# Kernel optimization log

Measured on AMD Instinct MI355X. Metric: run time of the kernel, lower is better.

## Reference

```python
import jax, jax.numpy as jnp
import numpy as np

N = 50000   # nodes
E = 800000  # edges (avg degree 16)
D = 64      # feature dim (input_dim == hidden_dim == output_dim for num_layer=2)
BN_EPS = 1e-5


def setup_inputs() -> dict:
    key = jax.random.key(0)
    ks = jax.random.split(key, 8)
    def lin_w(k, fan_in, fan_out):
        return jax.random.normal(k, (fan_in, fan_out), jnp.float32) / np.sqrt(fan_in).astype(np.float32)
    inp = {
        "x": jax.random.normal(ks[0], (N, D), jnp.float32),
        "edge_index": jax.random.randint(ks[1], (2, E), 0, N),
    }
    ki = 2
    for l in range(2):
        for s in ("a", "b"):
            inp[f"w{l}{s}"] = lin_w(ks[ki], D, D)
            inp[f"b{l}{s}"] = jnp.zeros((D,), jnp.float32)
            inp[f"g{l}{s}"] = jnp.ones((D,), jnp.float32)   # BN gamma
            inp[f"be{l}{s}"] = jnp.zeros((D,), jnp.float32)  # BN beta
            ki += 1
    inp["lin_w"] = lin_w(ks[6], 2 * D, D)  # JK cat of 2 layers -> 2D, final lin -> D
    inp["lin_b"] = jnp.zeros((D,), jnp.float32)
    return inp


def _bn(h, g, b):
    # BatchNorm1d in training mode: batch statistics over the node axis
    m = h.mean(axis=0)
    v = h.var(axis=0)
    return (h - m) * jax.lax.rsqrt(v + BN_EPS) * g + b


def _gin(h, src, dst, w1, b1, g1, be1, w2, b2, g2, be2):
    # GINConv with eps=0: (1+eps)*x_i + sum_{j->i} x_j, then MLP(Lin-BN-ReLU-Lin-BN-ReLU)
    agg = jax.ops.segment_sum(h[src], dst, num_segments=N) + h
    h = jax.nn.relu(_bn(agg @ w1 + b1, g1, be1))
    return jax.nn.relu(_bn(h @ w2 + b2, g2, be2))


def reference(x, edge_index, w0a, b0a, g0a, be0a, w0b, b0b, g0b, be0b,
              w1a, b1a, g1a, be1a, w1b, b1b, g1b, be1b, lin_w, lin_b):
    src, dst = edge_index[0], edge_index[1]
    h1 = _gin(x, src, dst, w0a, b0a, g0a, be0a, w0b, b0b, g0b, be0b)
    h2 = _gin(h1, src, dst, w1a, b1a, g1a, be1a, w1b, b1b, g1b, be1b)
    # JumpingKnowledge 'cat' over the conv outputs (res[1:]), then final linear
    return jnp.concatenate([h1, h2], axis=1) @ lin_w + lin_b
```

## Files before the change

kernel.cpp:

```cpp
#include <hip/hip_runtime.h>
#include <hip/hip_bf16.h>

#define NN 50000
#define NE 800000
#define BN_EPS 1e-5f
#define CHUNK 4096
#define NCH 196
#define NBK 196

typedef __attribute__((ext_vector_type(4))) float f32x4;
typedef __attribute__((ext_vector_type(8))) short s16x8;
typedef __attribute__((ext_vector_type(4))) short s16x4;

__device__ __forceinline__ float bf2f(__hip_bfloat16 v) { return __bfloat162float(v); }
__device__ __forceinline__ short f2bs(float v) {
    __hip_bfloat16 b = __float2bfloat16(v);
    return __builtin_bit_cast(short, b);
}

__global__ void prep_k(const int* __restrict__ dst, int* __restrict__ part,
                       const float* __restrict__ x, __hip_bfloat16* __restrict__ Xb,
                       const float* __restrict__ w0a, const float* __restrict__ w0b,
                       const float* __restrict__ w1a, const float* __restrict__ w1b,
                       const float* __restrict__ lw,
                       short* __restrict__ Wt0a, short* __restrict__ Wt0b,
                       short* __restrict__ Wt1a, short* __restrict__ Wt1b,
                       short* __restrict__ Wtf) {
    int b = blockIdx.x, t = threadIdx.x;
    if (b < NCH) {
        __shared__ int c[256];
        c[t] = 0;
        __syncthreads();
        int base = b * CHUNK;
        int n = NE - base; if (n > CHUNK) n = CHUNK;
        for (int i = t; i < n; i += 256) atomicAdd(&c[dst[base + i] >> 8], 1);
        __syncthreads();
        part[b * 256 + t] = c[t];
    } else if (b < 196 + 3125) {
        int i = (b - 196) * 256 + t;
        if (i < NN * 16) {
            f32x4 v = *(const f32x4*)(x + (size_t)i * 4);
            s16x4 ov;
            #pragma unroll
            for (int j = 0; j < 4; j++) ov[j] = f2bs(v[j]);
            *(s16x4*)((short*)Xb + (size_t)i * 4) = ov;
        }
    } else {
        int wb = b - 3321;
        if (wb < 4) {
            const float* W = wb == 0 ? w0a : wb == 1 ? w0b : wb == 2 ? w1a : w1b;
            short* Wt = wb == 0 ? Wt0a : wb == 1 ? Wt0b : wb == 2 ? Wt1a : Wt1b;
            for (int e = t; e < 4096; e += 256) {
                int k = e >> 6, n = e & 63;
                Wt[n * 64 + k] = f2bs(W[e]);
            }
        } else {
            for (int e = t; e < 8192; e += 256) {
                int k = e >> 6, n = e & 63;
                Wtf[n * 128 + k] = f2bs(lw[e]);
            }
        }
    }
}

__global__ void bscan_k(const int* __restrict__ part, int* __restrict__ bbase,
                        int* __restrict__ bres, int* __restrict__ off,
                        float* __restrict__ sums) {
    __shared__ int s[256];
    int t = threadIdx.x;
    int v = 0;
    for (int c = 0; c < NCH; c++) v += part[c * 256 + t];
    s[t] = v;
    __syncthreads();
    for (int d = 1; d < 256; d <<= 1) {
        int u = (t >= d) ? s[t - d] : 0;
        __syncthreads();
        s[t] += u;
        __syncthreads();
    }
    int ex = s[t] - v;
    bbase[t] = ex;
    bres[t] = ex;
    if (t == 0) { bbase[256] = NE; off[NN] = NE; }
    sums[t] = 0.f; sums[256 + t] = 0.f;
}

__global__ void bscatter_k(const int* __restrict__ src, const int* __restrict__ dst,
                           int* __restrict__ bres, int* __restrict__ ebuf) {
    __shared__ int cnt[256], loff[256], lcur[256], gst[256], sc[256];
    __shared__ int packed[CHUNK];
    int t = threadIdx.x;
    cnt[t] = 0;
    __syncthreads();
    int base = blockIdx.x * CHUNK;
    int n = NE - base; if (n > CHUNK) n = CHUNK;
    for (int i = t; i < n; i += 256) atomicAdd(&cnt[dst[base + i] >> 8], 1);
    __syncthreads();
    sc[t] = cnt[t];
    __syncthreads();
    for (int d = 1; d < 256; d <<= 1) {
        int u = (t >= d) ? sc[t - d] : 0;
        __syncthreads();
        sc[t] += u;
        __syncthreads();
    }
    loff[t] = sc[t] - cnt[t];
    lcur[t] = loff[t];
    __syncthreads();
    for (int i = t; i < n; i += 256) {
        int d = dst[base + i];
        int b = d >> 8;
        int p = atomicAdd(&lcur[b], 1);
        packed[p] = src[base + i] | ((d & 255) << 16) | (b << 24);
    }
    __syncthreads();
    if (cnt[t]) gst[t] = atomicAdd(&bres[t], cnt[t]);
    __syncthreads();
    for (int i = t; i < n; i += 256) {
        int v = packed[i];
        int b = (v >> 24) & 255;
        ebuf[gst[b] + i - loff[b]] = v & 0xFFFFFF;
    }
}

__global__ void csr_k(const int* __restrict__ bbase, const int* __restrict__ ebuf,
                      int* __restrict__ off, int* __restrict__ adj) {
    __shared__ int cnt[256], loff[256], lcur[256], sc[256];
    int b = blockIdx.x, t = threadIdx.x;
    int s0 = bbase[b], s1 = bbase[b + 1];
    int n = s1 - s0;
    cnt[t] = 0;
    __syncthreads();
    for (int i = t; i < n; i += 256) atomicAdd(&cnt[(ebuf[s0 + i] >> 16) & 255], 1);
    __syncthreads();
    sc[t] = cnt[t];
    __syncthreads();
    for (int d = 1; d < 256; d <<= 1) {
        int u = (t >= d) ? sc[t - d] : 0;
        __syncthreads();
        sc[t] += u;
        __syncthreads();
    }
    loff[t] = sc[t] - cnt[t];
    lcur[t] = loff[t];
    int node = b * 256 + t;
    if (node < NN) off[node] = s0 + loff[t];
    __syncthreads();
    for (int i = t; i < n; i += 256) {
        int v = ebuf[s0 + i];
        int p = atomicAdd(&lcur[(v >> 16) & 255], 1);
        adj[s0 + p] = v & 0xFFFF;
    }
}

__global__ void gather_k(const __hip_bfloat16* __restrict__ X,
                         const int* __restrict__ off, const int* __restrict__ adj,
                         __hip_bfloat16* __restrict__ AGG) {
    int node = blockIdx.x * 4 + (threadIdx.x >> 6);
    int lane = threadIdx.x & 63;
    if (node >= NN) return;
    float acc = bf2f(X[(size_t)node * 64 + lane]);
    int s = off[node], e = off[node + 1];
    int p = s;
    for (; p + 8 <= e; p += 8) {
        int j0 = adj[p + 0], j1 = adj[p + 1], j2 = adj[p + 2], j3 = adj[p + 3];
        int j4 = adj[p + 4], j5 = adj[p + 5], j6 = adj[p + 6], j7 = adj[p + 7];
        float v0 = bf2f(X[(size_t)j0 * 64 + lane]);
        float v1 = bf2f(X[(size_t)j1 * 64 + lane]);
        float v2 = bf2f(X[(size_t)j2 * 64 + lane]);
        float v3 = bf2f(X[(size_t)j3 * 64 + lane]);
        float v4 = bf2f(X[(size_t)j4 * 64 + lane]);
        float v5 = bf2f(X[(size_t)j5 * 64 + lane]);
        float v6 = bf2f(X[(size_t)j6 * 64 + lane]);
        float v7 = bf2f(X[(size_t)j7 * 64 + lane]);
        acc += ((v0 + v1) + (v2 + v3)) + ((v4 + v5) + (v6 + v7));
    }
    if (p + 4 <= e) {
        int j0 = adj[p + 0], j1 = adj[p + 1], j2 = adj[p + 2], j3 = adj[p + 3];
        float v0 = bf2f(X[(size_t)j0 * 64 + lane]);
        float v1 = bf2f(X[(size_t)j1 * 64 + lane]);
        float v2 = bf2f(X[(size_t)j2 * 64 + lane]);
        float v3 = bf2f(X[(size_t)j3 * 64 + lane]);
        acc += (v0 + v1) + (v2 + v3);
        p += 4;
    }
    for (; p < e; p++) acc += bf2f(X[(size_t)adj[p] * 64 + lane]);
    AGG[(size_t)node * 64 + lane] = __float2bfloat16(acc);
}


__global__ void gemm_a_k(const __hip_bfloat16* __restrict__ Ab,
                         const short* __restrict__ Wt,
                         const float* __restrict__ bias,
                         float* __restrict__ T,
                         float* __restrict__ sums) {
    __shared__ float lsum[64], lssq[64];
    int tid = threadIdx.x;
    if (tid < 64) { lsum[tid] = 0.f; lssq[tid] = 0.f; }
    __syncthreads();
    int wv = tid >> 6, L = tid & 63;
    int m = L & 15, quad = L >> 4;
    int wrow = blockIdx.x * 64 + wv * 16;
    int arow = wrow + m;
    if (arow >= NN) arow = NN - 1;
    const short* Ap = (const short*)Ab;
    s16x8 a0 = *(const s16x8*)(Ap + (size_t)arow * 64 + quad * 8);
    s16x8 a1 = *(const s16x8*)(Ap + (size_t)arow * 64 + 32 + quad * 8);
    f32x4 acc[4];
    #pragma unroll
    for (int nt = 0; nt < 4; nt++) {
        int n = nt * 16 + m;
        s16x8 b0 = *(const s16x8*)(Wt + n * 64 + quad * 8);
        s16x8 b1 = *(const s16x8*)(Wt + n * 64 + 32 + quad * 8);
        acc[nt] = (f32x4){0.f, 0.f, 0.f, 0.f};
        acc[nt] = __builtin_amdgcn_mfma_f32_16x16x32_bf16(a0, b0, acc[nt], 0, 0, 0);
        acc[nt] = __builtin_amdgcn_mfma_f32_16x16x32_bf16(a1, b1, acc[nt], 0, 0, 0);
    }
    #pragma unroll
    for (int nt = 0; nt < 4; nt++) {
        int col = nt * 16 + m;
        float bv = bias[col];
        float ps = 0.f, pq = 0.f;
        #pragma unroll
        for (int r = 0; r < 4; r++) {
            int orow = wrow + quad * 4 + r;
            if (orow < NN) {
                float v = acc[nt][r] + bv;
                T[(size_t)orow * 64 + col] = v;
                ps += v;
                pq += v * v;
            }
        }
        atomicAdd(&lsum[col], ps);
        atomicAdd(&lssq[col], pq);
    }
    __syncthreads();
    if (tid < 64) {
        atomicAdd(&sums[tid], lsum[tid]);
        atomicAdd(&sums[64 + tid], lssq[tid]);
    }
}

__global__ void gemm_bn_k(const float* __restrict__ Tin,
                          const float* __restrict__ stats,
                          const float* __restrict__ g, const float* __restrict__ be,
                          const short* __restrict__ Wt,
                          const float* __restrict__ bias,
                          float* __restrict__ T,
                          float* __restrict__ sums) {
    __shared__ float sc[64], sh[64], lsum[64], lssq[64];
    int tid = threadIdx.x;
    if (tid < 64) {
        float mm = stats[tid] * (1.0f / NN);
        float var = stats[64 + tid] * (1.0f / NN) - mm * mm;
        if (var < 0.f) var = 0.f;
        float s = g[tid] * rsqrtf(var + BN_EPS);
        sc[tid] = s;
        sh[tid] = be[tid] - mm * s;
        lsum[tid] = 0.f; lssq[tid] = 0.f;
    }
    __syncthreads();
    int wv = tid >> 6, L = tid & 63;
    int m = L & 15, quad = L >> 4;
    int wrow = blockIdx.x * 64 + wv * 16;
    int arow = wrow + m;
    if (arow >= NN) arow = NN - 1;
    f32x4 t0 = *(const f32x4*)(Tin + (size_t)arow * 64 + quad * 8);
    f32x4 t1 = *(const f32x4*)(Tin + (size_t)arow * 64 + quad * 8 + 4);
    f32x4 t2 = *(const f32x4*)(Tin + (size_t)arow * 64 + 32 + quad * 8);
    f32x4 t3 = *(const f32x4*)(Tin + (size_t)arow * 64 + 32 + quad * 8 + 4);
    s16x8 a0, a1;
    #pragma unroll
    for (int j = 0; j < 4; j++) {
        int k0 = quad * 8 + j, k1 = quad * 8 + 4 + j;
        float u0 = t0[j] * sc[k0] + sh[k0]; a0[j]     = f2bs(u0 > 0.f ? u0 : 0.f);
        float u1 = t1[j] * sc[k1] + sh[k1]; a0[4 + j] = f2bs(u1 > 0.f ? u1 : 0.f);
        float u2 = t2[j] * sc[32 + k0] + sh[32 + k0]; a1[j]     = f2bs(u2 > 0.f ? u2 : 0.f);
        float u3 = t3[j] * sc[32 + k1] + sh[32 + k1]; a1[4 + j] = f2bs(u3 > 0.f ? u3 : 0.f);
    }
    f32x4 acc[4];
    #pragma unroll
    for (int nt = 0; nt < 4; nt++) {
        int n = nt * 16 + m;
        s16x8 b0 = *(const s16x8*)(Wt + n * 64 + quad * 8);
        s16x8 b1 = *(const s16x8*)(Wt + n * 64 + 32 + quad * 8);
        acc[nt] = (f32x4){0.f, 0.f, 0.f, 0.f};
        acc[nt] = __builtin_amdgcn_mfma_f32_16x16x32_bf16(a0, b0, acc[nt], 0, 0, 0);
        acc[nt] = __builtin_amdgcn_mfma_f32_16x16x32_bf16(a1, b1, acc[nt], 0, 0, 0);
    }
    #pragma unroll
    for (int nt = 0; nt < 4; nt++) {
        int col = nt * 16 + m;
        float bv = bias[col];
        float ps = 0.f, pq = 0.f;
        #pragma unroll
        for (int r = 0; r < 4; r++) {
            int orow = wrow + quad * 4 + r;
            if (orow < NN) {
                float v = acc[nt][r] + bv;
                T[(size_t)orow * 64 + col] = v;
                ps += v;
                pq += v * v;
            }
        }
        atomicAdd(&lsum[col], ps);
        atomicAdd(&lssq[col], pq);
    }
    __syncthreads();
    if (tid < 64) {
        atomicAdd(&sums[tid], lsum[tid]);
        atomicAdd(&sums[64 + tid], lssq[tid]);
    }
}

__global__ void bn_k(const float* __restrict__ T, const float* __restrict__ sums,
                     const float* __restrict__ g, const float* __restrict__ be,
                     __hip_bfloat16* __restrict__ Hb) {
    __shared__ float sc[64], sh[64];
    int tid = threadIdx.x;
    if (tid < 64) {
        float m = sums[tid] * (1.0f / NN);
        float var = sums[64 + tid] * (1.0f / NN) - m * m;
        if (var < 0.f) var = 0.f;
        float s = g[tid] * rsqrtf(var + BN_EPS);
        sc[tid] = s;
        sh[tid] = be[tid] - m * s;
    }
    __syncthreads();
    int i = blockIdx.x * 256 + tid;
    if (i < NN * 16) {
        int row = i >> 4, f = (i & 15) * 4;
        f32x4 v = *(const f32x4*)(T + (size_t)row * 64 + f);
        s16x4 ub;
        #pragma unroll
        for (int j = 0; j < 4; j++) {
            float w = v[j] * sc[f + j] + sh[f + j];
            ub[j] = f2bs(w > 0.f ? w : 0.f);
        }
        *(s16x4*)((short*)Hb + (size_t)row * 64 + f) = ub;
    }
}

__global__ void gemm_fin_k(const __hip_bfloat16* __restrict__ H1b,
                           const float* __restrict__ T2,
                           const float* __restrict__ stats,
                           const float* __restrict__ g, const float* __restrict__ be,
                           const short* __restrict__ Wtf,
                           const float* __restrict__ bias,
                           float* __restrict__ O) {
    __shared__ float sc[64], sh[64];
    int tid = threadIdx.x;
    if (tid < 64) {
        float mm = stats[tid] * (1.0f / NN);
        float var = stats[64 + tid] * (1.0f / NN) - mm * mm;
        if (var < 0.f) var = 0.f;
        float s = g[tid] * rsqrtf(var + BN_EPS);
        sc[tid] = s;
        sh[tid] = be[tid] - mm * s;
    }
    __syncthreads();
    int wv = tid >> 6, L = tid & 63;
    int m = L & 15, quad = L >> 4;
    int wrow = blockIdx.x * 64 + wv * 16;
    int arow = wrow + m;
    if (arow >= NN) arow = NN - 1;
    const short* Hp = (const short*)H1b;
    s16x8 a0 = *(const s16x8*)(Hp + (size_t)arow * 64 + quad * 8);
    s16x8 a1 = *(const s16x8*)(Hp + (size_t)arow * 64 + 32 + quad * 8);
    f32x4 t0 = *(const f32x4*)(T2 + (size_t)arow * 64 + quad * 8);
    f32x4 t1 = *(const f32x4*)(T2 + (size_t)arow * 64 + quad * 8 + 4);
    f32x4 t2 = *(const f32x4*)(T2 + (size_t)arow * 64 + 32 + quad * 8);
    f32x4 t3 = *(const f32x4*)(T2 + (size_t)arow * 64 + 32 + quad * 8 + 4);
    s16x8 a2, a3;
    #pragma unroll
    for (int j = 0; j < 4; j++) {
        int k0 = quad * 8 + j, k1 = quad * 8 + 4 + j;
        float u0 = t0[j] * sc[k0] + sh[k0]; a2[j]     = f2bs(u0 > 0.f ? u0 : 0.f);
        float u1 = t1[j] * sc[k1] + sh[k1]; a2[4 + j] = f2bs(u1 > 0.f ? u1 : 0.f);
        float u2 = t2[j] * sc[32 + k0] + sh[32 + k0]; a3[j]     = f2bs(u2 > 0.f ? u2 : 0.f);
        float u3 = t3[j] * sc[32 + k1] + sh[32 + k1]; a3[4 + j] = f2bs(u3 > 0.f ? u3 : 0.f);
    }
    f32x4 acc[4];
    #pragma unroll
    for (int nt = 0; nt < 4; nt++) {
        int n = nt * 16 + m;
        s16x8 b0 = *(const s16x8*)(Wtf + n * 128 + quad * 8);
        s16x8 b1 = *(const s16x8*)(Wtf + n * 128 + 32 + quad * 8);
        s16x8 b2 = *(const s16x8*)(Wtf + n * 128 + 64 + quad * 8);
        s16x8 b3 = *(const s16x8*)(Wtf + n * 128 + 96 + quad * 8);
        acc[nt] = (f32x4){0.f, 0.f, 0.f, 0.f};
        acc[nt] = __builtin_amdgcn_mfma_f32_16x16x32_bf16(a0, b0, acc[nt], 0, 0, 0);
        acc[nt] = __builtin_amdgcn_mfma_f32_16x16x32_bf16(a1, b1, acc[nt], 0, 0, 0);
        acc[nt] = __builtin_amdgcn_mfma_f32_16x16x32_bf16(a2, b2, acc[nt], 0, 0, 0);
        acc[nt] = __builtin_amdgcn_mfma_f32_16x16x32_bf16(a3, b3, acc[nt], 0, 0, 0);
    }
    #pragma unroll
    for (int nt = 0; nt < 4; nt++) {
        int col = nt * 16 + m;
        float bv = bias[col];
        #pragma unroll
        for (int r = 0; r < 4; r++) {
            int orow = wrow + quad * 4 + r;
            if (orow < NN) O[(size_t)orow * 64 + col] = acc[nt][r] + bv;
        }
    }
}

extern "C" void kernel_launch(void* const* d_in, const int* in_sizes, int n_in,
                              void* d_out, int out_size, void* d_ws, size_t ws_size,
                              hipStream_t stream) {
    const float* x   = (const float*)d_in[0];
    const int*   ei  = (const int*)d_in[1];
    const float* w0a = (const float*)d_in[2];
    const float* b0a = (const float*)d_in[3];
    const float* g0a = (const float*)d_in[4];
    const float* be0a= (const float*)d_in[5];
    const float* w0b = (const float*)d_in[6];
    const float* b0b = (const float*)d_in[7];
    const float* g0b = (const float*)d_in[8];
    const float* be0b= (const float*)d_in[9];
    const float* w1a = (const float*)d_in[10];
    const float* b1a = (const float*)d_in[11];
    const float* g1a = (const float*)d_in[12];
    const float* be1a= (const float*)d_in[13];
    const float* w1b = (const float*)d_in[14];
    const float* b1b = (const float*)d_in[15];
    const float* g1b = (const float*)d_in[16];
    const float* be1b= (const float*)d_in[17];
    const float* lw  = (const float*)d_in[18];
    const float* lb  = (const float*)d_in[19];
    float* out = (float*)d_out;
    (void)in_sizes; (void)n_in; (void)out_size; (void)ws_size;

    char* wsb = (char*)d_ws;
    size_t o = 0;
    auto alloc = [&](size_t bytes) -> char* {
        char* p = wsb + o;
        o += (bytes + 255) & ~(size_t)255;
        return p;
    };
    int* part = (int*)alloc(NCH * 256 * 4);
    float* sums = (float*)alloc(512 * 4);
    int* bbase = (int*)alloc(257 * 4);
    int* bres = (int*)alloc(256 * 4);
    int* off = (int*)alloc((NN + 1) * 4);
    int* adj = (int*)alloc(NE * 4);
    int* ebuf = (int*)alloc(NE * 4);
    __hip_bfloat16* Xb   = (__hip_bfloat16*)alloc((size_t)NN * 64 * 2);
    __hip_bfloat16* AGGb = (__hip_bfloat16*)alloc((size_t)NN * 64 * 2);
    __hip_bfloat16* HCb  = (__hip_bfloat16*)alloc((size_t)NN * 64 * 2);
    float* T  = (float*)alloc((size_t)NN * 64 * 4);
    float* T2 = (float*)alloc((size_t)NN * 64 * 4);
    short* Wt0a = (short*)alloc(4096 * 2);
    short* Wt0b = (short*)alloc(4096 * 2);
    short* Wt1a = (short*)alloc(4096 * 2);
    short* Wt1b = (short*)alloc(4096 * 2);
    short* Wtf  = (short*)alloc(8192 * 2);

    const int* src = ei;
    const int* dst = ei + NE;

    prep_k<<<3326, 256, 0, stream>>>(dst, part, x, Xb, w0a, w0b, w1a, w1b, lw,
                                     Wt0a, Wt0b, Wt1a, Wt1b, Wtf);
    bscan_k<<<1, 256, 0, stream>>>(part, bbase, bres, off, sums);
    bscatter_k<<<NCH, 256, 0, stream>>>(src, dst, bres, ebuf);
    csr_k<<<NBK, 256, 0, stream>>>(bbase, ebuf, off, adj);

    const int ggrid = NN / 4;
    const int mgrid = (NN + 63) / 64;
    const int agrid = (NN * 16 + 255) / 256;

    gather_k<<<ggrid, 256, 0, stream>>>(Xb, off, adj, AGGb);
    gemm_a_k<<<mgrid, 256, 0, stream>>>(AGGb, Wt0a, b0a, T, sums + 0);
    gemm_bn_k<<<mgrid, 256, 0, stream>>>(T, sums + 0, g0a, be0a, Wt0b, b0b, T2, sums + 128);
    bn_k<<<agrid, 256, 0, stream>>>(T2, sums + 128, g0b, be0b, HCb);

    gather_k<<<ggrid, 256, 0, stream>>>(HCb, off, adj, AGGb);
    gemm_a_k<<<mgrid, 256, 0, stream>>>(AGGb, Wt1a, b1a, T, sums + 256);
    gemm_bn_k<<<mgrid, 256, 0, stream>>>(T, sums + 256, g1a, be1a, Wt1b, b1b, T2, sums + 384);

    gemm_fin_k<<<mgrid, 256, 0, stream>>>(HCb, T2, sums + 384, g1b, be1b, Wtf, lb, out);
}
```

Before: 348.3 us.

## Fuse all pipeline stages into one cooperative persistent kernel with grid syncs

```diff
diff --git a/kernel.cpp b/kernel.cpp
--- a/kernel.cpp
+++ b/kernel.cpp
@@ -1,12 +1,17 @@
 #include <hip/hip_runtime.h>
 #include <hip/hip_bf16.h>
+#include <hip/hip_cooperative_groups.h>
+
+namespace cg = cooperative_groups;
 
 #define NN 50000
 #define NE 800000
 #define BN_EPS 1e-5f
 #define CHUNK 4096
 #define NCH 196
-#define NBK 196
+#define GRID 512
+#define PREPV (NCH + 3125 + 5)
+#define MGRID 782
 
 typedef __attribute__((ext_vector_type(4))) float f32x4;
 typedef __attribute__((ext_vector_type(8))) short s16x8;
@@ -18,38 +23,54 @@
     return __builtin_bit_cast(short, b);
 }
 
-__global__ void prep_k(const int* __restrict__ dst, int* __restrict__ part,
-                       const float* __restrict__ x, __hip_bfloat16* __restrict__ Xb,
-                       const float* __restrict__ w0a, const float* __restrict__ w0b,
-                       const float* __restrict__ w1a, const float* __restrict__ w1b,
-                       const float* __restrict__ lw,
-                       short* __restrict__ Wt0a, short* __restrict__ Wt0b,
-                       short* __restrict__ Wt1a, short* __restrict__ Wt1b,
-                       short* __restrict__ Wtf) {
-    int b = blockIdx.x, t = threadIdx.x;
-    if (b < NCH) {
-        __shared__ int c[256];
-        c[t] = 0;
-        __syncthreads();
-        int base = b * CHUNK;
+struct P {
+    const int* src; const int* dst;
+    int* part; float* sums;
+    int* bbase; int* bres; int* off; int* adj; int* ebuf;
+    const float* x;
+    __hip_bfloat16* Xb; __hip_bfloat16* AGGb; __hip_bfloat16* HCb;
+    float* T; float* T2;
+    const float *w0a, *w0b, *w1a, *w1b, *lw;
+    short *Wt0a, *Wt0b, *Wt1a, *Wt1b, *Wtf;
+    const float *b0a, *g0a, *be0a, *b0b, *g0b, *be0b;
+    const float *b1a, *g1a, *be1a, *b1b, *g1b, *be1b;
+    const float* lb;
+    float* out;
+};
+
+union SMem {
+    int hist_c[256];
+    int scan_s[256];
+    struct { int cnt[256], loff[256], lcur[256], gst[256], sc[256]; int packed[CHUNK]; } sca;
+    struct { float sc[64], sh[64], lsum[64], lssq[64]; } bn;
+};
+
+
+__device__ __forceinline__ void stage_prep(int vb, int t, SMem& u, const P& p) {
+    if (vb < NCH) {
+        __syncthreads();
+        u.hist_c[t] = 0;
+        __syncthreads();
+        int base = vb * CHUNK;
         int n = NE - base; if (n > CHUNK) n = CHUNK;
-        for (int i = t; i < n; i += 256) atomicAdd(&c[dst[base + i] >> 8], 1);
-        __syncthreads();
-        part[b * 256 + t] = c[t];
-    } else if (b < 196 + 3125) {
-        int i = (b - 196) * 256 + t;
+        for (int i = t; i < n; i += 256) atomicAdd(&u.hist_c[p.dst[base + i] >> 8], 1);
+        __syncthreads();
+        p.part[vb * 256 + t] = u.hist_c[t];
+        __syncthreads();
+    } else if (vb < NCH + 3125) {
+        int i = (vb - NCH) * 256 + t;
         if (i < NN * 16) {
-            f32x4 v = *(const f32x4*)(x + (size_t)i * 4);
+            f32x4 v = *(const f32x4*)(p.x + (size_t)i * 4);
             s16x4 ov;
             #pragma unroll
             for (int j = 0; j < 4; j++) ov[j] = f2bs(v[j]);
-            *(s16x4*)((short*)Xb + (size_t)i * 4) = ov;
+            *(s16x4*)((short*)p.Xb + (size_t)i * 4) = ov;
         }
     } else {
-        int wb = b - 3321;
+        int wb = vb - (NCH + 3125);
         if (wb < 4) {
-            const float* W = wb == 0 ? w0a : wb == 1 ? w0b : wb == 2 ? w1a : w1b;
-            short* Wt = wb == 0 ? Wt0a : wb == 1 ? Wt0b : wb == 2 ? Wt1a : Wt1b;
+            const float* W = wb == 0 ? p.w0a : wb == 1 ? p.w0b : wb == 2 ? p.w1a : p.w1b;
+            short* Wt = wb == 0 ? p.Wt0a : wb == 1 ? p.Wt0b : wb == 2 ? p.Wt1a : p.Wt1b;
             for (int e = t; e < 4096; e += 256) {
                 int k = e >> 6, n = e & 63;
                 Wt[n * 64 + k] = f2bs(W[e]);
@@ -57,108 +78,99 @@
         } else {
             for (int e = t; e < 8192; e += 256) {
                 int k = e >> 6, n = e & 63;
-                Wtf[n * 128 + k] = f2bs(lw[e]);
+                p.Wtf[n * 128 + k] = f2bs(p.lw[e]);
             }
         }
     }
 }
 
-__global__ void bscan_k(const int* __restrict__ part, int* __restrict__ bbase,
-                        int* __restrict__ bres, int* __restrict__ off,
-                        float* __restrict__ sums) {
-    __shared__ int s[256];
-    int t = threadIdx.x;
+__device__ __forceinline__ void stage_scan(int t, SMem& u, const P& p) {
     int v = 0;
-    for (int c = 0; c < NCH; c++) v += part[c * 256 + t];
-    s[t] = v;
+    for (int c = 0; c < NCH; c++) v += p.part[c * 256 + t];
+    u.scan_s[t] = v;
     __syncthreads();
     for (int d = 1; d < 256; d <<= 1) {
-        int u = (t >= d) ? s[t - d] : 0;
-        __syncthreads();
-        s[t] += u;
-        __syncthreads();
-    }
-    int ex = s[t] - v;
-    bbase[t] = ex;
-    bres[t] = ex;
-    if (t == 0) { bbase[256] = NE; off[NN] = NE; }
-    sums[t] = 0.f; sums[256 + t] = 0.f;
-}
-
-__global__ void bscatter_k(const int* __restrict__ src, const int* __restrict__ dst,
-                           int* __restrict__ bres, int* __restrict__ ebuf) {
-    __shared__ int cnt[256], loff[256], lcur[256], gst[256], sc[256];
-    __shared__ int packed[CHUNK];
-    int t = threadIdx.x;
-    cnt[t] = 0;
-    __syncthreads();
-    int base = blockIdx.x * CHUNK;
+        int uu = (t >= d) ? u.scan_s[t - d] : 0;
+        __syncthreads();
+        u.scan_s[t] += uu;
+        __syncthreads();
+    }
+    int ex = u.scan_s[t] - v;
+    p.bbase[t] = ex;
+    p.bres[t] = ex;
+    if (t == 0) { p.bbase[256] = NE; p.off[NN] = NE; }
+    p.sums[t] = 0.f;
+    p.sums[256 + t] = 0.f;
+}
+
+__device__ __forceinline__ void stage_scatter(int vb, int t, SMem& u, const P& p) {
+    __syncthreads();
+    u.sca.cnt[t] = 0;
+    __syncthreads();
+    int base = vb * CHUNK;
     int n = NE - base; if (n > CHUNK) n = CHUNK;
-    for (int i = t; i < n; i += 256) atomicAdd(&cnt[dst[base + i] >> 8], 1);
-    __syncthreads();
-    sc[t] = cnt[t];
+    for (int i = t; i < n; i += 256) atomicAdd(&u.sca.cnt[p.dst[base + i] >> 8], 1);
+    __syncthreads();
+    u.sca.sc[t] = u.sca.cnt[t];
     __syncthreads();
     for (int d = 1; d < 256; d <<= 1) {
-        int u = (t >= d) ? sc[t - d] : 0;
-        __syncthreads();
-        sc[t] += u;
-        __syncthreads();
-    }
-    loff[t] = sc[t] - cnt[t];
-    lcur[t] = loff[t];
+        int uu = (t >= d) ? u.sca.sc[t - d] : 0;
+        __syncthreads();
+        u.sca.sc[t] += uu;
+        __syncthreads();
+    }
+    u.sca.loff[t] = u.sca.sc[t] - u.sca.cnt[t];
+    u.sca.lcur[t] = u.sca.loff[t];
     __syncthreads();
     for (int i = t; i < n; i += 256) {
-        int d = dst[base + i];
-        int b = d >> 8;
-        int p = atomicAdd(&lcur[b], 1);
-        packed[p] = src[base + i] | ((d & 255) << 16) | (b << 24);
-    }
-    __syncthreads();
-    if (cnt[t]) gst[t] = atomicAdd(&bres[t], cnt[t]);
+        int d = p.dst[base + i];
+        int bk = d >> 8;
+        int pos = atomicAdd(&u.sca.lcur[bk], 1);
+        u.sca.packed[pos] = p.src[base + i] | ((d & 255) << 16) | (bk << 24);
+    }
+    __syncthreads();
+    if (u.sca.cnt[t]) u.sca.gst[t] = atomicAdd(&p.bres[t], u.sca.cnt[t]);
     __syncthreads();
     for (int i = t; i < n; i += 256) {
-        int v = packed[i];
-        int b = (v >> 24) & 255;
-        ebuf[gst[b] + i - loff[b]] = v & 0xFFFFFF;
-    }
-}
-
-__global__ void csr_k(const int* __restrict__ bbase, const int* __restrict__ ebuf,
-                      int* __restrict__ off, int* __restrict__ adj) {
-    __shared__ int cnt[256], loff[256], lcur[256], sc[256];
-    int b = blockIdx.x, t = threadIdx.x;
-    int s0 = bbase[b], s1 = bbase[b + 1];
+        int v = u.sca.packed[i];
+        int bk = (v >> 24) & 255;
+        p.ebuf[u.sca.gst[bk] + i - u.sca.loff[bk]] = v & 0xFFFFFF;
+    }
+    __syncthreads();
+}
+
+__device__ __forceinline__ void stage_csr(int vb, int t, SMem& u, const P& p) {
+    __syncthreads();
+    int s0 = p.bbase[vb], s1 = p.bbase[vb + 1];
     int n = s1 - s0;
-    cnt[t] = 0;
-    __syncthreads();
-    for (int i = t; i < n; i += 256) atomicAdd(&cnt[(ebuf[s0 + i] >> 16) & 255], 1);
-    __syncthreads();
-    sc[t] = cnt[t];
+    u.sca.cnt[t] = 0;
+    __syncthreads();
+    for (int i = t; i < n; i += 256) atomicAdd(&u.sca.cnt[(p.ebuf[s0 + i] >> 16) & 255], 1);
+    __syncthreads();
+    u.sca.sc[t] = u.sca.cnt[t];
     __syncthreads();
     for (int d = 1; d < 256; d <<= 1) {
-        int u = (t >= d) ? sc[t - d] : 0;
-        __syncthreads();
-        sc[t] += u;
-        __syncthreads();
-    }
-    loff[t] = sc[t] - cnt[t];
-    lcur[t] = loff[t];
-    int node = b * 256 + t;
-    if (node < NN) off[node] = s0 + loff[t];
+        int uu = (t >= d) ? u.sca.sc[t - d] : 0;
+        __syncthreads();
+        u.sca.sc[t] += uu;
+        __syncthreads();
+    }
+    u.sca.loff[t] = u.sca.sc[t] - u.sca.cnt[t];
+    u.sca.lcur[t] = u.sca.loff[t];
+    int node = vb * 256 + t;
+    if (node < NN) p.off[node] = s0 + u.sca.loff[t];
     __syncthreads();
     for (int i = t; i < n; i += 256) {
-        int v = ebuf[s0 + i];
-        int p = atomicAdd(&lcur[(v >> 16) & 255], 1);
-        adj[s0 + p] = v & 0xFFFF;
-    }
-}
-
-__global__ void gather_k(const __hip_bfloat16* __restrict__ X,
-                         const int* __restrict__ off, const int* __restrict__ adj,
-                         __hip_bfloat16* __restrict__ AGG) {
-    int node = blockIdx.x * 4 + (threadIdx.x >> 6);
-    int lane = threadIdx.x & 63;
-    if (node >= NN) return;
+        int v = p.ebuf[s0 + i];
+        int pos = atomicAdd(&u.sca.lcur[(v >> 16) & 255], 1);
+        p.adj[s0 + pos] = v & 0xFFFF;
+    }
+    __syncthreads();
+}
+
+__device__ __forceinline__ float gather_row(const __hip_bfloat16* __restrict__ X,
+                                            int lane, const int* __restrict__ off,
+                                            const int* __restrict__ adj, int node) {
     float acc = bf2f(X[(size_t)node * 64 + lane]);
     int s = off[node], e = off[node + 1];
     int p = s;
@@ -185,22 +197,32 @@
         p += 4;
     }
     for (; p < e; p++) acc += bf2f(X[(size_t)adj[p] * 64 + lane]);
-    AGG[(size_t)node * 64 + lane] = __float2bfloat16(acc);
-}
-
-
-__global__ void gemm_a_k(const __hip_bfloat16* __restrict__ Ab,
-                         const short* __restrict__ Wt,
-                         const float* __restrict__ bias,
-                         float* __restrict__ T,
-                         float* __restrict__ sums) {
-    __shared__ float lsum[64], lssq[64];
-    int tid = threadIdx.x;
-    if (tid < 64) { lsum[tid] = 0.f; lssq[tid] = 0.f; }
-    __syncthreads();
-    int wv = tid >> 6, L = tid & 63;
+    return acc;
+}
+
+__device__ __forceinline__ void bn_coeff(int t, const float* __restrict__ stats,
+                                         const float* __restrict__ g,
+                                         const float* __restrict__ be,
+                                         float* sc, float* sh) {
+    if (t < 64) {
+        float m = stats[t] * (1.0f / NN);
+        float var = stats[64 + t] * (1.0f / NN) - m * m;
+        if (var < 0.f) var = 0.f;
+        float s = g[t] * rsqrtf(var + BN_EPS);
+        sc[t] = s;
+        sh[t] = be[t] - m * s;
+    }
+}
+
+__device__ __forceinline__ void stage_gemm_a(int B, int t, const __hip_bfloat16* Ab,
+                                             const short* Wt, const float* bias,
+                                             float* T, float* sums, SMem& u) {
+    __syncthreads();
+    if (t < 64) { u.bn.lsum[t] = 0.f; u.bn.lssq[t] = 0.f; }
+    __syncthreads();
+    int wv = t >> 6, L = t & 63;
     int m = L & 15, quad = L >> 4;
-    int wrow = blockIdx.x * 64 + wv * 16;
+    int wrow = B * 64 + wv * 16;
     int arow = wrow + m;
     if (arow >= NN) arow = NN - 1;
     const short* Ap = (const short*)Ab;
@@ -231,38 +253,28 @@
                 pq += v * v;
             }
         }
-        atomicAdd(&lsum[col], ps);
-        atomicAdd(&lssq[col], pq);
-    }
-    __syncthreads();
-    if (tid < 64) {
-        atomicAdd(&sums[tid], lsum[tid]);
-        atomicAdd(&sums[64 + tid], lssq[tid]);
-    }
-}
-
-__global__ void gemm_bn_k(const float* __restrict__ Tin,
-                          const float* __restrict__ stats,
-                          const float* __restrict__ g, const float* __restrict__ be,
-                          const short* __restrict__ Wt,
-                          const float* __restrict__ bias,
-                          float* __restrict__ T,
-                          float* __restrict__ sums) {
-    __shared__ float sc[64], sh[64], lsum[64], lssq[64];
-    int tid = threadIdx.x;
-    if (tid < 64) {
-        float mm = stats[tid] * (1.0f / NN);
-        float var = stats[64 + tid] * (1.0f / NN) - mm * mm;
-        if (var < 0.f) var = 0.f;
-        float s = g[tid] * rsqrtf(var + BN_EPS);
-        sc[tid] = s;
-        sh[tid] = be[tid] - mm * s;
-        lsum[tid] = 0.f; lssq[tid] = 0.f;
-    }
-    __syncthreads();
-    int wv = tid >> 6, L = tid & 63;
+        atomicAdd(&u.bn.lsum[col], ps);
+        atomicAdd(&u.bn.lssq[col], pq);
+    }
+    __syncthreads();
+    if (t < 64) {
+        atomicAdd(&sums[t], u.bn.lsum[t]);
+        atomicAdd(&sums[64 + t], u.bn.lssq[t]);
+    }
+}
+
+__device__ __forceinline__ void stage_gemm_bn(int B, int t, const float* Tin,
+                                              const float* stats, const float* g,
+                                              const float* be, const short* Wt,
+                                              const float* bias, float* T, float* sums,
+                                              SMem& u) {
+    __syncthreads();
+    bn_coeff(t, stats, g, be, u.bn.sc, u.bn.sh);
+    if (t < 64) { u.bn.lsum[t] = 0.f; u.bn.lssq[t] = 0.f; }
+    __syncthreads();
+    int wv = t >> 6, L = t & 63;
     int m = L & 15, quad = L >> 4;
-    int wrow = blockIdx.x * 64 + wv * 16;
+    int wrow = B * 64 + wv * 16;
     int arow = wrow + m;
     if (arow >= NN) arow = NN - 1;
     f32x4 t0 = *(const f32x4*)(Tin + (size_t)arow * 64 + quad * 8);
@@ -273,10 +285,10 @@
     #pragma unroll
     for (int j = 0; j < 4; j++) {
         int k0 = quad * 8 + j, k1 = quad * 8 + 4 + j;
-        float u0 = t0[j] * sc[k0] + sh[k0]; a0[j]     = f2bs(u0 > 0.f ? u0 : 0.f);
-        float u1 = t1[j] * sc[k1] + sh[k1]; a0[4 + j] = f2bs(u1 > 0.f ? u1 : 0.f);
-        float u2 = t2[j] * sc[32 + k0] + sh[32 + k0]; a1[j]     = f2bs(u2 > 0.f ? u2 : 0.f);
-        float u3 = t3[j] * sc[32 + k1] + sh[32 + k1]; a1[4 + j] = f2bs(u3 > 0.f ? u3 : 0.f);
+        float u0 = t0[j] * u.bn.sc[k0] + u.bn.sh[k0]; a0[j]     = f2bs(u0 > 0.f ? u0 : 0.f);
+        float u1 = t1[j] * u.bn.sc[k1] + u.bn.sh[k1]; a0[4 + j] = f2bs(u1 > 0.f ? u1 : 0.f);
+        float u2 = t2[j] * u.bn.sc[32 + k0] + u.bn.sh[32 + k0]; a1[j]     = f2bs(u2 > 0.f ? u2 : 0.f);
+        float u3 = t3[j] * u.bn.sc[32 + k1] + u.bn.sh[32 + k1]; a1[4 + j] = f2bs(u3 > 0.f ? u3 : 0.f);
     }
     f32x4 acc[4];
     #pragma unroll
@@ -303,91 +315,46 @@
                 pq += v * v;
             }
         }
-        atomicAdd(&lsum[col], ps);
-        atomicAdd(&lssq[col], pq);
-    }
-    __syncthreads();
-    if (tid < 64) {
-        atomicAdd(&sums[tid], lsum[tid]);
-        atomicAdd(&sums[64 + tid], lssq[tid]);
-    }
-}
-
-__global__ void bn_k(const float* __restrict__ T, const float* __restrict__ sums,
-                     const float* __restrict__ g, const float* __restrict__ be,
-                     __hip_bfloat16* __restrict__ Hb) {
-    __shared__ float sc[64], sh[64];
-    int tid = threadIdx.x;
-    if (tid < 64) {
-        float m = sums[tid] * (1.0f / NN);
-        float var = sums[64 + tid] * (1.0f / NN) - m * m;
-        if (var < 0.f) var = 0.f;
-        float s = g[tid] * rsqrtf(var + BN_EPS);
-        sc[tid] = s;
-        sh[tid] = be[tid] - m * s;
-    }
-    __syncthreads();
-    int i = blockIdx.x * 256 + tid;
-    if (i < NN * 16) {
-        int row = i >> 4, f = (i & 15) * 4;
-        f32x4 v = *(const f32x4*)(T + (size_t)row * 64 + f);
-        s16x4 ub;
-        #pragma unroll
-        for (int j = 0; j < 4; j++) {
-            float w = v[j] * sc[f + j] + sh[f + j];
-            ub[j] = f2bs(w > 0.f ? w : 0.f);
-        }
-        *(s16x4*)((short*)Hb + (size_t)row * 64 + f) = ub;
-    }
-}
-
-__global__ void gemm_fin_k(const __hip_bfloat16* __restrict__ H1b,
-                           const float* __restrict__ T2,
-                           const float* __restrict__ stats,
-                           const float* __restrict__ g, const float* __restrict__ be,
-                           const short* __restrict__ Wtf,
-                           const float* __restrict__ bias,
-                           float* __restrict__ O) {
-    __shared__ float sc[64], sh[64];
-    int tid = threadIdx.x;
-    if (tid < 64) {
-        float mm = stats[tid] * (1.0f / NN);
-        float var = stats[64 + tid] * (1.0f / NN) - mm * mm;
-        if (var < 0.f) var = 0.f;
-        float s = g[tid] * rsqrtf(var + BN_EPS);
-        sc[tid] = s;
-        sh[tid] = be[tid] - mm * s;
-    }
-    __syncthreads();
-    int wv = tid >> 6, L = tid & 63;
+        atomicAdd(&u.bn.lsum[col], ps);
+        atomicAdd(&u.bn.lssq[col], pq);
+    }
+    __syncthreads();
+    if (t < 64) {
+        atomicAdd(&sums[t], u.bn.lsum[t]);
+        atomicAdd(&sums[64 + t], u.bn.lssq[t]);
+    }
+}
+
+__device__ __forceinline__ void stage_fin(int B, int t, SMem& u, const P& p) {
+    int wv = t >> 6, L = t & 63;
     int m = L & 15, quad = L >> 4;
-    int wrow = blockIdx.x * 64 + wv * 16;
+    int wrow = B * 64 + wv * 16;
     int arow = wrow + m;
     if (arow >= NN) arow = NN - 1;
-    const short* Hp = (const short*)H1b;
+    const short* Hp = (const short*)p.HCb;
     s16x8 a0 = *(const s16x8*)(Hp + (size_t)arow * 64 + quad * 8);
     s16x8 a1 = *(const s16x8*)(Hp + (size_t)arow * 64 + 32 + quad * 8);
-    f32x4 t0 = *(const f32x4*)(T2 + (size_t)arow * 64 + quad * 8);
-    f32x4 t1 = *(const f32x4*)(T2 + (size_t)arow * 64 + quad * 8 + 4);
-    f32x4 t2 = *(const f32x4*)(T2 + (size_t)arow * 64 + 32 + quad * 8);
-    f32x4 t3 = *(const f32x4*)(T2 + (size_t)arow * 64 + 32 + quad * 8 + 4);
+    f32x4 t0 = *(const f32x4*)(p.T2 + (size_t)arow * 64 + quad * 8);
+    f32x4 t1 = *(const f32x4*)(p.T2 + (size_t)arow * 64 + quad * 8 + 4);
+    f32x4 t2 = *(const f32x4*)(p.T2 + (size_t)arow * 64 + 32 + quad * 8);
+    f32x4 t3 = *(const f32x4*)(p.T2 + (size_t)arow * 64 + 32 + quad * 8 + 4);
     s16x8 a2, a3;
     #pragma unroll
     for (int j = 0; j < 4; j++) {
         int k0 = quad * 8 + j, k1 = quad * 8 + 4 + j;
-        float u0 = t0[j] * sc[k0] + sh[k0]; a2[j]     = f2bs(u0 > 0.f ? u0 : 0.f);
-        float u1 = t1[j] * sc[k1] + sh[k1]; a2[4 + j] = f2bs(u1 > 0.f ? u1 : 0.f);
-        float u2 = t2[j] * sc[32 + k0] + sh[32 + k0]; a3[j]     = f2bs(u2 > 0.f ? u2 : 0.f);
-        float u3 = t3[j] * sc[32 + k1] + sh[32 + k1]; a3[4 + j] = f2bs(u3 > 0.f ? u3 : 0.f);
+        float u0 = t0[j] * u.bn.sc[k0] + u.bn.sh[k0]; a2[j]     = f2bs(u0 > 0.f ? u0 : 0.f);
+        float u1 = t1[j] * u.bn.sc[k1] + u.bn.sh[k1]; a2[4 + j] = f2bs(u1 > 0.f ? u1 : 0.f);
+        float u2 = t2[j] * u.bn.sc[32 + k0] + u.bn.sh[32 + k0]; a3[j]     = f2bs(u2 > 0.f ? u2 : 0.f);
+        float u3 = t3[j] * u.bn.sc[32 + k1] + u.bn.sh[32 + k1]; a3[4 + j] = f2bs(u3 > 0.f ? u3 : 0.f);
     }
     f32x4 acc[4];
     #pragma unroll
     for (int nt = 0; nt < 4; nt++) {
         int n = nt * 16 + m;
-        s16x8 b0 = *(const s16x8*)(Wtf + n * 128 + quad * 8);
-        s16x8 b1 = *(const s16x8*)(Wtf + n * 128 + 32 + quad * 8);
-        s16x8 b2 = *(const s16x8*)(Wtf + n * 128 + 64 + quad * 8);
-        s16x8 b3 = *(const s16x8*)(Wtf + n * 128 + 96 + quad * 8);
+        s16x8 b0 = *(const s16x8*)(p.Wtf + n * 128 + quad * 8);
+        s16x8 b1 = *(const s16x8*)(p.Wtf + n * 128 + 32 + quad * 8);
+        s16x8 b2 = *(const s16x8*)(p.Wtf + n * 128 + 64 + quad * 8);
+        s16x8 b3 = *(const s16x8*)(p.Wtf + n * 128 + 96 + quad * 8);
         acc[nt] = (f32x4){0.f, 0.f, 0.f, 0.f};
         acc[nt] = __builtin_amdgcn_mfma_f32_16x16x32_bf16(a0, b0, acc[nt], 0, 0, 0);
         acc[nt] = __builtin_amdgcn_mfma_f32_16x16x32_bf16(a1, b1, acc[nt], 0, 0, 0);
@@ -397,87 +364,196 @@
     #pragma unroll
     for (int nt = 0; nt < 4; nt++) {
         int col = nt * 16 + m;
-        float bv = bias[col];
+        float bv = p.lb[col];
         #pragma unroll
         for (int r = 0; r < 4; r++) {
             int orow = wrow + quad * 4 + r;
-            if (orow < NN) O[(size_t)orow * 64 + col] = acc[nt][r] + bv;
-        }
-    }
+            if (orow < NN) p.out[(size_t)orow * 64 + col] = acc[nt][r] + bv;
+        }
+    }
+}
+
+__global__ void __launch_bounds__(256) fused_k(P p) {
+    cg::grid_group grid = cg::this_grid();
+    __shared__ SMem u;
+    int B = blockIdx.x, t = threadIdx.x, G = gridDim.x;
+    int lane = t & 63, wv = t >> 6;
+
+    for (int vb = B; vb < PREPV; vb += G) stage_prep(vb, t, u, p);
+    grid.sync();
+    if (B == 0) stage_scan(t, u, p);
+    grid.sync();
+    for (int vb = B; vb < NCH; vb += G) stage_scatter(vb, t, u, p);
+    grid.sync();
+    for (int vb = B; vb < NCH; vb += G) stage_csr(vb, t, u, p);
+    grid.sync();
+    for (int vb = B; vb < 12500; vb += G) {
+        int node = vb * 4 + wv;
+        if (node < NN) {
+            float acc = gather_row(p.Xb, lane, p.off, p.adj, node);
+            p.AGGb[(size_t)node * 64 + lane] = __float2bfloat16(acc);
+        }
+    }
+    grid.sync();
+    for (int vb = B; vb < MGRID; vb += G)
+        stage_gemm_a(vb, t, p.AGGb, p.Wt0a, p.b0a, p.T, p.sums + 0, u);
+    grid.sync();
+    for (int vb = B; vb < MGRID; vb += G)
+        stage_gemm_bn(vb, t, p.T, p.sums + 0, p.g0a, p.be0a, p.Wt0b, p.b0b,
+                      p.T2, p.sums + 128, u);
+    grid.sync();
+    __syncthreads();
+    bn_coeff(t, p.sums + 128, p.g0b, p.be0b, u.bn.sc, u.bn.sh);
+    __syncthreads();
+    for (int vb = B; vb < 3125; vb += G) {
+        int i = vb * 256 + t;
+        if (i < NN * 16) {
+            int row = i >> 4, f = (i & 15) * 4;
+            f32x4 v = *(const f32x4*)(p.T2 + (size_t)row * 64 + f);
+            s16x4 ub;
+            #pragma unroll
+            for (int j = 0; j < 4; j++) {
+                float w = v[j] * u.bn.sc[f + j] + u.bn.sh[f + j];
+                ub[j] = f2bs(w > 0.f ? w : 0.f);
+            }
+            *(s16x4*)((short*)p.HCb + (size_t)row * 64 + f) = ub;
+        }
+    }
+    grid.sync();
+    for (int vb = B; vb < 12500; vb += G) {
+        int node = vb * 4 + wv;
+        if (node < NN) {
+            float acc = gather_row(p.HCb, lane, p.off, p.adj, node);
+            p.AGGb[(size_t)node * 64 + lane] = __float2bfloat16(acc);
+        }
+    }
+    grid.sync();
+    for (int vb = B; vb < MGRID; vb += G)
+        stage_gemm_a(vb, t, p.AGGb, p.Wt1a, p.b1a, p.T, p.sums + 256, u);
+    grid.sync();
+    for (int vb = B; vb < MGRID; vb += G)
+        stage_gemm_bn(vb, t, p.T, p.sums + 256, p.g1a, p.be1a, p.Wt1b, p.b1b,
+                      p.T2, p.sums + 384, u);
+    grid.sync();
+    __syncthreads();
+    bn_coeff(t, p.sums + 384, p.g1b, p.be1b, u.bn.sc, u.bn.sh);
+    __syncthreads();
+    for (int vb = B; vb < MGRID; vb += G) stage_fin(vb, t, u, p);
+}
+
+__global__ void prep_w(P p)  { __shared__ SMem u; stage_prep(blockIdx.x, threadIdx.x, u, p); }
+__global__ void scan_w(P p)  { __shared__ SMem u; stage_scan(threadIdx.x, u, p); }
+__global__ void scat_w(P p)  { __shared__ SMem u; stage_scatter(blockIdx.x, threadIdx.x, u, p); }
+__global__ void csrb_w(P p)  { __shared__ SMem u; stage_csr(blockIdx.x, threadIdx.x, u, p); }
+__global__ void gath_w(P p, int layer) {
+    int node = blockIdx.x * 4 + (threadIdx.x >> 6);
+    int lane = threadIdx.x & 63;
+    if (node >= NN) return;
+    const __hip_bfloat16* X = layer == 0 ? p.Xb : p.HCb;
+    float acc = gather_row(X, lane, p.off, p.adj, node);
+    p.AGGb[(size_t)node * 64 + lane] = __float2bfloat16(acc);
+}
+__global__ void gemma_w(P p, int layer) {
+    __shared__ SMem u;
+    if (layer == 0) stage_gemm_a(blockIdx.x, threadIdx.x, p.AGGb, p.Wt0a, p.b0a, p.T, p.sums + 0, u);
+    else            stage_gemm_a(blockIdx.x, threadIdx.x, p.AGGb, p.Wt1a, p.b1a, p.T, p.sums + 256, u);
+}
+__global__ void gemmbn_w(P p, int layer) {
+    __shared__ SMem u;
+    if (layer == 0) stage_gemm_bn(blockIdx.x, threadIdx.x, p.T, p.sums + 0, p.g0a, p.be0a,
+                                  p.Wt0b, p.b0b, p.T2, p.sums + 128, u);
+    else            stage_gemm_bn(blockIdx.x, threadIdx.x, p.T, p.sums + 256, p.g1a, p.be1a,
+                                  p.Wt1b, p.b1b, p.T2, p.sums + 384, u);
+}
+__global__ void bnfin_w(P p) {
+    __shared__ SMem u;
+    int t = threadIdx.x;
+    bn_coeff(t, p.sums + 128, p.g0b, p.be0b, u.bn.sc, u.bn.sh);
+    __syncthreads();
+    int i = blockIdx.x * 256 + t;
+    if (i < NN * 16) {
+        int row = i >> 4, f = (i & 15) * 4;
+        f32x4 v = *(const f32x4*)(p.T2 + (size_t)row * 64 + f);
+        s16x4 ub;
+        #pragma unroll
+        for (int j = 0; j < 4; j++) {
+            float w = v[j] * u.bn.sc[f + j] + u.bn.sh[f + j];
+            ub[j] = f2bs(w > 0.f ? w : 0.f);
+        }
+        *(s16x4*)((short*)p.HCb + (size_t)row * 64 + f) = ub;
+    }
+}
+__global__ void fin_w(P p) {
+    __shared__ SMem u;
+    int t = threadIdx.x;
+    bn_coeff(t, p.sums + 384, p.g1b, p.be1b, u.bn.sc, u.bn.sh);
+    __syncthreads();
+    stage_fin(blockIdx.x, t, u, p);
 }
 
 extern "C" void kernel_launch(void* const* d_in, const int* in_sizes, int n_in,
                               void* d_out, int out_size, void* d_ws, size_t ws_size,
                               hipStream_t stream) {
-    const float* x   = (const float*)d_in[0];
-    const int*   ei  = (const int*)d_in[1];
-    const float* w0a = (const float*)d_in[2];
-    const float* b0a = (const float*)d_in[3];
-    const float* g0a = (const float*)d_in[4];
-    const float* be0a= (const float*)d_in[5];
-    const float* w0b = (const float*)d_in[6];
-    const float* b0b = (const float*)d_in[7];
-    const float* g0b = (const float*)d_in[8];
-    const float* be0b= (const float*)d_in[9];
-    const float* w1a = (const float*)d_in[10];
-    const float* b1a = (const float*)d_in[11];
-    const float* g1a = (const float*)d_in[12];
-    const float* be1a= (const float*)d_in[13];
-    const float* w1b = (const float*)d_in[14];
-    const float* b1b = (const float*)d_in[15];
-    const float* g1b = (const float*)d_in[16];
-    const float* be1b= (const float*)d_in[17];
-    const float* lw  = (const float*)d_in[18];
-    const float* lb  = (const float*)d_in[19];
-    float* out = (float*)d_out;
     (void)in_sizes; (void)n_in; (void)out_size; (void)ws_size;
+    const int* ei = (const int*)d_in[1];
 
     char* wsb = (char*)d_ws;
     size_t o = 0;
     auto alloc = [&](size_t bytes) -> char* {
-        char* p = wsb + o;
+        char* ptr = wsb + o;
         o += (bytes + 255) & ~(size_t)255;
-        return p;
+        return ptr;
     };
-    int* part = (int*)alloc(NCH * 256 * 4);
-    float* sums = (float*)alloc(512 * 4);
-    int* bbase = (int*)alloc(257 * 4);
-    int* bres = (int*)alloc(256 * 4);
-    int* off = (int*)alloc((NN + 1) * 4);
-    int* adj = (int*)alloc(NE * 4);
-    int* ebuf = (int*)alloc(NE * 4);
-    __hip_bfloat16* Xb   = (__hip_bfloat16*)alloc((size_t)NN * 64 * 2);
-    __hip_bfloat16* AGGb = (__hip_bfloat16*)alloc((size_t)NN * 64 * 2);
-    __hip_bfloat16* HCb  = (__hip_bfloat16*)alloc((size_t)NN * 64 * 2);
-    float* T  = (float*)alloc((size_t)NN * 64 * 4);
-    float* T2 = (float*)alloc((size_t)NN * 64 * 4);
-    short* Wt0a = (short*)alloc(4096 * 2);
-    short* Wt0b = (short*)alloc(4096 * 2);
-    short* Wt1a = (short*)alloc(4096 * 2);
-    short* Wt1b = (short*)alloc(4096 * 2);
-    short* Wtf  = (short*)alloc(8192 * 2);
-
-    const int* src = ei;
-    const int* dst = ei + NE;
-
-    prep_k<<<3326, 256, 0, stream>>>(dst, part, x, Xb, w0a, w0b, w1a, w1b, lw,
-                                     Wt0a, Wt0b, Wt1a, Wt1b, Wtf);
-    bscan_k<<<1, 256, 0, stream>>>(part, bbase, bres, off, sums);
-    bscatter_k<<<NCH, 256, 0, stream>>>(src, dst, bres, ebuf);
-    csr_k<<<NBK, 256, 0, stream>>>(bbase, ebuf, off, adj);
-
-    const int ggrid = NN / 4;
-    const int mgrid = (NN + 63) / 64;
-    const int agrid = (NN * 16 + 255) / 256;
-
-    gather_k<<<ggrid, 256, 0, stream>>>(Xb, off, adj, AGGb);
-    gemm_a_k<<<mgrid, 256, 0, stream>>>(AGGb, Wt0a, b0a, T, sums + 0);
-    gemm_bn_k<<<mgrid, 256, 0, stream>>>(T, sums + 0, g0a, be0a, Wt0b, b0b, T2, sums + 128);
-    bn_k<<<agrid, 256, 0, stream>>>(T2, sums + 128, g0b, be0b, HCb);
-
-    gather_k<<<ggrid, 256, 0, stream>>>(HCb, off, adj, AGGb);
-    gemm_a_k<<<mgrid, 256, 0, stream>>>(AGGb, Wt1a, b1a, T, sums + 256);
-    gemm_bn_k<<<mgrid, 256, 0, stream>>>(T, sums + 256, g1a, be1a, Wt1b, b1b, T2, sums + 384);
-
-    gemm_fin_k<<<mgrid, 256, 0, stream>>>(HCb, T2, sums + 384, g1b, be1b, Wtf, lb, out);
-}
+
+    P p;
+    p.src = ei;
+    p.dst = ei + NE;
+    p.part  = (int*)alloc(NCH * 256 * 4);
+    p.sums  = (float*)alloc(512 * 4);
+    p.bbase = (int*)alloc(257 * 4);
+    p.bres  = (int*)alloc(256 * 4);
+    p.off   = (int*)alloc((NN + 1) * 4);
+    p.adj   = (int*)alloc(NE * 4);
+    p.ebuf  = (int*)alloc(NE * 4);
+    p.Xb    = (__hip_bfloat16*)alloc((size_t)NN * 64 * 2);
+    p.AGGb  = (__hip_bfloat16*)alloc((size_t)NN * 64 * 2);
+    p.HCb   = (__hip_bfloat16*)alloc((size_t)NN * 64 * 2);
+    p.T     = (float*)alloc((size_t)NN * 64 * 4);
+    p.T2    = (float*)alloc((size_t)NN * 64 * 4);
+    p.Wt0a  = (short*)alloc(4096 * 2);
+    p.Wt0b  = (short*)alloc(4096 * 2);
+    p.Wt1a  = (short*)alloc(4096 * 2);
+    p.Wt1b  = (short*)alloc(4096 * 2);
+    p.Wtf   = (short*)alloc(8192 * 2);
+
+    p.x   = (const float*)d_in[0];
+    p.w0a = (const float*)d_in[2];  p.b0a = (const float*)d_in[3];
+    p.g0a = (const float*)d_in[4];  p.be0a = (const float*)d_in[5];
+    p.w0b = (const float*)d_in[6];  p.b0b = (const float*)d_in[7];
+    p.g0b = (const float*)d_in[8];  p.be0b = (const float*)d_in[9];
+    p.w1a = (const float*)d_in[10]; p.b1a = (const float*)d_in[11];
+    p.g1a = (const float*)d_in[12]; p.be1a = (const float*)d_in[13];
+    p.w1b = (const float*)d_in[14]; p.b1b = (const float*)d_in[15];
+    p.g1b = (const float*)d_in[16]; p.be1b = (const float*)d_in[17];
+    p.lw  = (const float*)d_in[18]; p.lb = (const float*)d_in[19];
+    p.out = (float*)d_out;
+
+    void* args[] = { &p };
+    hipError_t err = hipLaunchCooperativeKernel(reinterpret_cast<void*>(fused_k),
+                                                dim3(GRID), dim3(256), args, 0, stream);
+    if (err != hipSuccess) {
+        (void)hipGetLastError();
+        prep_w  <<<PREPV, 256, 0, stream>>>(p);
+        scan_w  <<<1,     256, 0, stream>>>(p);
+        scat_w  <<<NCH,   256, 0, stream>>>(p);
+        csrb_w  <<<NCH,   256, 0, stream>>>(p);
+        gath_w  <<<12500, 256, 0, stream>>>(p, 0);
+        gemma_w <<<MGRID, 256, 0, stream>>>(p, 0);
+        gemmbn_w<<<MGRID, 256, 0, stream>>>(p, 0);
+        bnfin_w <<<3125,  256, 0, stream>>>(p);
+        gath_w  <<<12500, 256, 0, stream>>>(p, 1);
+        gemma_w <<<MGRID, 256, 0, stream>>>(p, 1);
+        gemmbn_w<<<MGRID, 256, 0, stream>>>(p, 1);
+        fin_w   <<<MGRID, 256, 0, stream>>>(p);
+    }
+}
```

Result: slower. 979.2 us (+181.1%).
